# Performance work log

Hardware: AMD Instinct MI355X
Metric: run time of the kernel (lower is better)

## Reference

```python
import jax, jax.numpy as jnp
import numpy as np

B, C, Ci, H, W = 4, 256, 128, 64, 64  # batch, in_channels, inter_channels, spatial
BN_EPS = 1e-5


def setup_inputs() -> dict:
    key = jax.random.key(0)
    ks = jax.random.split(key, 8)
    s = (2.0 / C) ** 0.5  # kaiming fan_in std for 1x1 conv over C inputs
    return {
        "a": jax.random.normal(ks[0], (B, C, H, W), jnp.float32),
        "b": jax.random.normal(ks[1], (B, C, H, W), jnp.float32),
        "theta_w": jax.random.normal(ks[2], (Ci, C), jnp.float32) * s,
        "theta_b": jnp.zeros((Ci,), jnp.float32),
        "phi_w": jax.random.normal(ks[3], (Ci, C), jnp.float32) * s,
        "phi_b": jnp.zeros((Ci,), jnp.float32),
        "g_w": jax.random.normal(ks[4], (Ci, C), jnp.float32) * s,
        "g_b": jnp.zeros((Ci,), jnp.float32),
        "W_w": jax.random.normal(ks[5], (C, Ci), jnp.float32) * (2.0 / Ci) ** 0.5,
        "bn_gamma": jnp.ones((C,), jnp.float32),
        "bn_beta": jnp.zeros((C,), jnp.float32),
        "bn_mean": jnp.zeros((C,), jnp.float32),
        "bn_var": jnp.ones((C,), jnp.float32),
    }


def _conv1x1(x, w, bias=None):
    # x: [B,Cin,H,W], w: [Cout,Cin] -> [B,Cout,H,W]
    y = jnp.einsum("oc,bchw->bohw", w, x)
    if bias is not None:
        y = y + bias[None, :, None, None]
    return y


def reference(a, b, theta_w, theta_b, phi_w, phi_b, g_w, g_b, W_w,
              bn_gamma, bn_beta, bn_mean, bn_var):
    Bsz, _, h, w = a.shape
    n = h * w
    theta_a = _conv1x1(a, theta_w, theta_b).reshape(Bsz, Ci, n).transpose(0, 2, 1)  # [B,N,Ci]
    phi_b_ = _conv1x1(b, phi_w, phi_b).reshape(Bsz, Ci, n)                          # [B,Ci,N]
    f = jnp.einsum("bnc,bcm->bnm", theta_a, phi_b_) / n                             # [B,N,N]
    g_b_ = _conv1x1(b, g_w, g_b).reshape(Bsz, Ci, n).transpose(0, 2, 1)             # [B,N,Ci]
    y = jnp.einsum("bnm,bmc->bnc", f, g_b_)                                         # [B,N,Ci]
    y = y.transpose(0, 2, 1).reshape(Bsz, Ci, h, w)
    wy = _conv1x1(y, W_w)                                                           # no bias
    inv = jax.lax.rsqrt(bn_var + BN_EPS)
    out = (wy - bn_mean[None, :, None, None]) * (bn_gamma * inv)[None, :, None, None] \
          + bn_beta[None, :, None, None]
    return out
```

## Files before the change

### kernel.cpp

```cpp
#include <hip/hip_runtime.h>
#include <hip/hip_bf16.h>

#define NSP 4096
#define CCH 256
#define CIN 128
#define BN_EPS 1e-5f

typedef __bf16 bf16x8 __attribute__((ext_vector_type(8)));
typedef __bf16 bf16x4 __attribute__((ext_vector_type(4)));
typedef float f32x4 __attribute__((ext_vector_type(4)));
typedef unsigned short u16x8 __attribute__((ext_vector_type(8)));

typedef const __attribute__((address_space(1))) unsigned int gu32;
typedef __attribute__((address_space(3))) unsigned int lu32;


__device__ __forceinline__ float4 fetch_tr(const float* __restrict__ A, int lda, int m0,
                                           int k0, int tid) {
  const int r = tid >> 2, kq = (tid & 3) << 2;
  return *(const float4*)(A + (size_t)(m0 + r) * lda + k0 + kq);
}
__device__ __forceinline__ void stash_tr(float (*As)[68], float4 v, int tid) {
  const int r = tid >> 2, kq = (tid & 3) << 2;
  As[kq + 0][r] = v.x; As[kq + 1][r] = v.y; As[kq + 2][r] = v.z; As[kq + 3][r] = v.w;
}
__device__ __forceinline__ float4 fetch_dir(const float* __restrict__ B, int ldb, int k0,
                                            int n0, int tid) {
  const int kr = tid >> 4, nq = (tid & 15) << 2;
  return *(const float4*)(B + (size_t)(k0 + kr) * ldb + n0 + nq);
}
__device__ __forceinline__ void stash_dir(float (*Bs)[68], float4 v, int tid) {
  const int kr = tid >> 4, nq = (tid & 15) << 2;
  *(float4*)(&Bs[kr][nq]) = v;
}

__device__ __forceinline__ void mm16(const float (*As)[68], const float (*Bs)[68],
                                     float acc[4][4], int ty, int tx) {
#pragma unroll
  for (int kk = 0; kk < 16; ++kk) {
    const float4 av = *(const float4*)(&As[kk][ty << 2]);
    const float4 bv = *(const float4*)(&Bs[kk][tx << 2]);
    const float ar[4] = {av.x, av.y, av.z, av.w};
    const float br[4] = {bv.x, bv.y, bv.z, bv.w};
#pragma unroll
    for (int i = 0; i < 4; ++i)
#pragma unroll
      for (int j = 0; j < 4; ++j) acc[i][j] += ar[i] * br[j];
  }
}

__device__ __forceinline__ float wave_reduce(float v) {
#pragma unroll
  for (int off = 32; off; off >>= 1) v += __shfl_down(v, off);
  return v;
}

__global__ __launch_bounds__(256) void prep_kernel(
    const float* __restrict__ bin, const float* __restrict__ a,
    const float* __restrict__ W_w, const float* __restrict__ g_w,
    const float* __restrict__ phi_w, const float* __restrict__ theta_w,
    const float* __restrict__ phi_b, const float* __restrict__ theta_b,
    const float* __restrict__ g_b,
    __bf16* __restrict__ bhi, __bf16* __restrict__ blo,
    float* __restrict__ srow,
    float* __restrict__ Wg, __bf16* __restrict__ Wghi, __bf16* __restrict__ Wglo,
    __bf16* __restrict__ PTthi, __bf16* __restrict__ PTtlo,
    __bf16* __restrict__ at,
    float* __restrict__ vb_g, float* __restrict__ vpt, float* __restrict__ wgb,
    float* __restrict__ dvec) {
  __shared__ float smem[64 * 68];
  const int idx = blockIdx.x;
  const int t = threadIdx.x;
  const int wave = t >> 6, lane = t & 63;
  if (idx < 1024) {
    const int row = idx;
    const float* src = bin + (size_t)row * NSP + t * 16;
    float sum = 0.f;
    unsigned short h16[16], l16[16];
#pragma unroll
    for (int i = 0; i < 4; ++i) {
      const float4 v = *(const float4*)(src + i * 4);
      const float vv[4] = {v.x, v.y, v.z, v.w};
      sum += v.x + v.y + v.z + v.w;
#pragma unroll
      for (int e = 0; e < 4; ++e) {
        const unsigned u = __float_as_uint(vv[e]);
        h16[i * 4 + e] = (unsigned short)(u >> 16);
        const float hf = __uint_as_float(u & 0xffff0000u);
        l16[i * 4 + e] = (unsigned short)(__float_as_uint(vv[e] - hf) >> 16);
      }
    }
    unsigned short* dh = (unsigned short*)bhi + (size_t)row * NSP + t * 16;
    unsigned short* dl = (unsigned short*)blo + (size_t)row * NSP + t * 16;
    *(u16x8*)dh = *(u16x8*)&h16[0];
    *(u16x8*)(dh + 8) = *(u16x8*)&h16[8];
    *(u16x8*)dl = *(u16x8*)&l16[0];
    *(u16x8*)(dl + 8) = *(u16x8*)&l16[8];
#pragma unroll
    for (int off = 32; off; off >>= 1) sum += __shfl_down(sum, off);
    if (lane == 0) smem[wave] = sum;
    __syncthreads();
    if (t == 0) srow[row] = smem[0] + smem[1] + smem[2] + smem[3];
  } else if (idx < 2048) {
    const int p = idx - 1024;
    const int n0 = (p & 63) * 64, c0 = ((p >> 6) & 3) * 64, b = p >> 8;
    float (*tile)[68] = (float(*)[68])smem;
    const int cr = t >> 4, nq = (t & 15) << 2;
    const float* src = a + ((size_t)(b * CCH + c0)) * NSP + n0;
#pragma unroll
    for (int s = 0; s < 4; ++s) {
      const float4 v = *(const float4*)(src + (size_t)(cr + s * 16) * NSP + nq);
      *(float4*)&tile[cr + s * 16][nq] = v;
    }
    __syncthreads();
    const int n = t >> 2, cq = (t & 3) << 4;
    __bf16 outv[16];
#pragma unroll
    for (int i = 0; i < 16; ++i) outv[i] = (__bf16)tile[cq + i][n];
    __bf16* dst = at + ((size_t)(b * NSP + n0 + n)) * CCH + c0 + cq;
    *(bf16x8*)dst = *(bf16x8*)&outv[0];
    *(bf16x8*)(dst + 8) = *(bf16x8*)&outv[8];
  } else if (idx < 2080) {
    const int p = idx - 2048;
    const int zsel = p >> 4, rem = p & 15;
    const int m0 = (rem >> 2) * 64, n0 = (rem & 3) * 64;
    float (*As)[68] = (float(*)[68])smem;
    float (*Bs)[68] = (float(*)[68])(smem + 16 * 68);
    const int ty = t >> 4, tx = t & 15;
    float acc[4][4] = {};
    if (zsel == 0) {
      float4 ar = fetch_tr(W_w, CIN, m0, 0, t);
      float4 br = fetch_dir(g_w, CCH, 0, n0, t);
      for (int kt = 0; kt < 8; ++kt) {
        stash_tr(As, ar, t); stash_dir(Bs, br, t);
        __syncthreads();
        if (kt < 7) { ar = fetch_tr(W_w, CIN, m0, (kt + 1) * 16, t);
                      br = fetch_dir(g_w, CCH, (kt + 1) * 16, n0, t); }
        mm16(As, Bs, acc, ty, tx);
        __syncthreads();
      }
#pragma unroll
      for (int i = 0; i < 4; ++i) {
        const size_t off = (size_t)(m0 + (ty << 2) + i) * 256 + n0 + (tx << 2);
        *(float4*)(Wg + off) = make_float4(acc[i][0], acc[i][1], acc[i][2], acc[i][3]);
        __bf16 h4[4], l4[4];
#pragma unroll
        for (int j = 0; j < 4; ++j) {
          const __bf16 h = (__bf16)acc[i][j];
          h4[j] = h; l4[j] = (__bf16)(acc[i][j] - (float)h);
        }
        *(bf16x4*)(Wghi + off) = *(bf16x4*)h4;
        *(bf16x4*)(Wglo + off) = *(bf16x4*)l4;
      }
    } else {
      float4 ar = fetch_dir(theta_w, CCH, 0, m0, t);
      float4 br = fetch_dir(phi_w, CCH, 0, n0, t);
      for (int kt = 0; kt < 8; ++kt) {
        stash_dir(As, ar, t); stash_dir(Bs, br, t);
        __syncthreads();
        if (kt < 7) { ar = fetch_dir(theta_w, CCH, (kt + 1) * 16, m0, t);
                      br = fetch_dir(phi_w, CCH, (kt + 1) * 16, n0, t); }
        mm16(As, Bs, acc, ty, tx);
        __syncthreads();
      }
#pragma unroll
      for (int i = 0; i < 4; ++i) {
        const size_t off = (size_t)(m0 + (ty << 2) + i) * 256 + n0 + (tx << 2);
        __bf16 h4[4], l4[4];
#pragma unroll
        for (int j = 0; j < 4; ++j) {
          const __bf16 h = (__bf16)acc[i][j];
          h4[j] = h; l4[j] = (__bf16)(acc[i][j] - (float)h);
        }
        *(bf16x4*)(PTthi + off) = *(bf16x4*)h4;
        *(bf16x4*)(PTtlo + off) = *(bf16x4*)l4;
      }
    }
  } else if (idx == 2080) {
    float* tb_s = smem;
    float* pb_s = smem + 128;
    if (t < 128) { tb_s[t] = theta_b[t]; pb_s[t] = phi_b[t]; }
    __syncthreads();
    float acc = 0.f;
#pragma unroll 8
    for (int i = 0; i < 128; ++i) acc += phi_w[(size_t)i * 256 + t] * tb_s[i];
    vb_g[t] = acc;
    if (t < 64) {
      float pv = pb_s[t] * tb_s[t] + pb_s[t + 64] * tb_s[t + 64];
      pv = wave_reduce(pv);
      if (t == 0) dvec[0] = pv;
    }
  } else if (idx == 2081) {
    float* pb_s = smem;
    if (t < 128) pb_s[t] = phi_b[t];
    __syncthreads();
    float acc = 0.f;
#pragma unroll 8
    for (int i = 0; i < 128; ++i) acc += pb_s[i] * theta_w[(size_t)i * 256 + t];
    vpt[t] = acc;
  } else {
    const int p = idx - 2082;
    float* gb_s = smem;
    if (t < 128) gb_s[t] = g_b[t];
    __syncthreads();
    const float2 gv = *(const float2*)&gb_s[lane * 2];
    for (int i = 0; i < 16; ++i) {
      const int o = p * 64 + wave * 16 + i;
      const float2 r = *(const float2*)(W_w + (size_t)o * 128 + lane * 2);
      float v = fmaf(r.x, gv.x, r.y * gv.y);
      v = wave_reduce(v);
      if (lane == 0) wgb[o] = v;
    }
  }
}

__global__ __launch_bounds__(256) void gram_kernel(
    const __bf16* __restrict__ bhi, const __bf16* __restrict__ blo,
    float* __restrict__ Gpart,
    const float* __restrict__ srow, const float* __restrict__ Wg,
    const __bf16* __restrict__ PTthi, const __bf16* __restrict__ PTtlo,
    const float* __restrict__ vb_g,
    float* __restrict__ Wgs, float* __restrict__ sPTv, float* __restrict__ dvec) {
  __shared__ __bf16 At[2][64][64];
  __shared__ __bf16 Bt[2][64][64];
  const int idx = blockIdx.x;
  const int t = threadIdx.x;
  const int wave = t >> 6, lane = t & 63;
  if (idx < 512) {
    const int jt = idx & 3, it = (idx >> 2) & 3;
    const int z = idx >> 4, batch = z >> 3, kc = z & 7;
    const int m = lane & 15, q = lane >> 4;
    const size_t rowbase = (size_t)batch * CCH;
    const int colbase = kc * 512;
    const int rseg = lane >> 3, ch = lane & 7;
    const int u = ch ^ rseg;
    const int h = u >> 2, j = u & 3;
    const __bf16* gsrc = h ? blo : bhi;

    auto stage = [&](int ph, int ks) {
#pragma unroll
      for (int c = 0; c < 4; ++c) {
        const int s = wave * 4 + c;
        const int isB = s >> 3;
        const int kb = s & 7;
        const int grow = (isB ? jt : it) * 64 + kb * 8 + rseg;
        const __bf16* gp = gsrc + (rowbase + (size_t)grow) * NSP +
                           colbase + ks * 32 + j * 8;
        const __bf16* lp = isB ? &Bt[ph][kb * 8][0] : &At[ph][kb * 8][0];
        __builtin_amdgcn_global_load_lds((gu32*)(const void*)gp,
                                         (lu32*)(void*)lp, 16, 0, 0);
      }
    };

    f32x4 acc[4] = {};
    const int chA = q ^ (m & 7);
    stage(0, 0);
    int ph = 0;
    for (int ks = 0; ks < 16; ++ks) {
      __syncthreads();
      if (ks < 15) stage(ph ^ 1, ks + 1);
      const bf16x8 ah = *(const bf16x8*)&At[ph][wave * 16 + m][chA * 8];
      const bf16x8 al = *(const bf16x8*)&At[ph][wave * 16 + m][(chA ^ 4) * 8];
#pragma unroll
      for (int t4 = 0; t4 < 4; ++t4) {
        const bf16x8 bh = *(const bf16x8*)&Bt[ph][t4 * 16 + m][chA * 8];
        const bf16x8 bl = *(const bf16x8*)&Bt[ph][t4 * 16 + m][(chA ^ 4) * 8];
        acc[t4] = __builtin_amdgcn_mfma_f32_16x16x32_bf16(ah, bh, acc[t4], 0, 0, 0);
        acc[t4] = __builtin_amdgcn_mfma_f32_16x16x32_bf16(ah, bl, acc[t4], 0, 0, 0);
        acc[t4] = __builtin_amdgcn_mfma_f32_16x16x32_bf16(al, bh, acc[t4], 0, 0, 0);
      }
      ph ^= 1;
    }
    float* Gp = Gpart + ((size_t)(kc * 4 + batch)) * 65536;
#pragma unroll
    for (int t4 = 0; t4 < 4; ++t4)
#pragma unroll
      for (int r = 0; r < 4; ++r)
        Gp[(size_t)(it * 64 + wave * 16 + q * 4 + r) * 256 + jt * 64 + t4 * 16 + m] =
            acc[t4][r];
  } else {
    float* lds = (float*)&At[0][0][0];
    const int p = idx - 512;
    const int b = p >> 4, seg = p & 15;
    lds[t] = srow[b * 256 + t];
    __syncthreads();
    const float4 sv = *(const float4*)&lds[lane * 4];
    for (int i = wave; i < 16; i += 4) {
      const int o = seg * 16 + i;
      const float4 r = *(const float4*)(Wg + (size_t)o * 256 + lane * 4);
      float v = fmaf(r.x, sv.x, fmaf(r.y, sv.y, fmaf(r.z, sv.z, r.w * sv.w)));
      v = wave_reduce(v);
      if (lane == 0) Wgs[b * 256 + o] = v;
    }
    for (int i = wave; i < 16; i += 4) {
      const int c = seg * 16 + i;
      const bf16x4 ph = *(const bf16x4*)(PTthi + (size_t)c * 256 + lane * 4);
      const bf16x4 pl = *(const bf16x4*)(PTtlo + (size_t)c * 256 + lane * 4);
      const float svv[4] = {sv.x, sv.y, sv.z, sv.w};
      float v = 0.f;
#pragma unroll
      for (int e = 0; e < 4; ++e) v += ((float)ph[e] + (float)pl[e]) * svv[e];
      v = wave_reduce(v);
      if (lane == 0) sPTv[b * 256 + c] = v;
    }
    if (seg == 0 && wave == 0) {
      const float4 vbv = *(const float4*)(vb_g + lane * 4);
      float v = fmaf(vbv.x, sv.x, fmaf(vbv.y, sv.y, fmaf(vbv.z, sv.z, vbv.w * sv.w)));
      v = wave_reduce(v);
      if (lane == 0) dvec[1 + b] = v;
    }
  }
}

__global__ __launch_bounds__(256) void redw2_kernel(
    const float* __restrict__ Gpart, const float* __restrict__ vb_g,
    float* __restrict__ t2_g,
    const __bf16* __restrict__ Wghi, const __bf16* __restrict__ Wglo,
    __bf16* __restrict__ W2hi, __bf16* __restrict__ W2lo) {
  const int blk = blockIdx.x;
  const int t = threadIdx.x;
  const int wave = t >> 6, lane = t & 63;
  __shared__ __bf16 Gsh[16][264], Gsl[16][264];
  const int b = blk >> 4, nt = blk & 15;
  const int rr = t >> 4;
  const int c0 = (t & 15) * 16;
  f32x4 s[4] = {};
#pragma unroll
  for (int p = 0; p < 8; ++p) {
    const float* src = Gpart + (((size_t)(p * 4 + b)) << 16) +
                       (size_t)(nt * 16 + rr) * 256 + c0;
#pragma unroll
    for (int e = 0; e < 4; ++e) s[e] += *(const f32x4*)(src + e * 4);
  }
  {
    float part = 0.f;
#pragma unroll
    for (int e = 0; e < 4; ++e) {
      const float4 vv = *(const float4*)(vb_g + c0 + e * 4);
      part += s[e][0] * vv.x + s[e][1] * vv.y + s[e][2] * vv.z + s[e][3] * vv.w;
    }
#pragma unroll
    for (int off = 8; off; off >>= 1) part += __shfl_down(part, off);
    if ((t & 15) == 0) t2_g[b * 256 + nt * 16 + rr] = part;
  }
  __bf16 h8[16], l8[16];
#pragma unroll
  for (int e = 0; e < 16; ++e) {
    const float x = s[e >> 2][e & 3];
    const __bf16 h = (__bf16)x;
    h8[e] = h; l8[e] = (__bf16)(x - (float)h);
  }
  *(bf16x8*)&Gsh[rr][c0] = *(bf16x8*)&h8[0];
  *(bf16x8*)&Gsh[rr][c0 + 8] = *(bf16x8*)&h8[8];
  *(bf16x8*)&Gsl[rr][c0] = *(bf16x8*)&l8[0];
  *(bf16x8*)&Gsl[rr][c0 + 8] = *(bf16x8*)&l8[8];
  __syncthreads();
  const int m = lane & 15, q = lane >> 4;
  f32x4 acc[4] = {};
#pragma unroll
  for (int ks = 0; ks < 8; ++ks) {
    const int k = ks * 32 + q * 8;
    const bf16x8 bh = *(const bf16x8*)&Gsh[m][k];
    const bf16x8 bl = *(const bf16x8*)&Gsl[m][k];
#pragma unroll
    for (int i = 0; i < 4; ++i) {
      const int mt = i * 4 + wave;
      const bf16x8 ah = *(const bf16x8*)(Wghi + (size_t)(mt * 16 + m) * 256 + k);
      const bf16x8 al = *(const bf16x8*)(Wglo + (size_t)(mt * 16 + m) * 256 + k);
      acc[i] = __builtin_amdgcn_mfma_f32_16x16x32_bf16(ah, bh, acc[i], 0, 0, 0);
      acc[i] = __builtin_amdgcn_mfma_f32_16x16x32_bf16(ah, bl, acc[i], 0, 0, 0);
      acc[i] = __builtin_amdgcn_mfma_f32_16x16x32_bf16(al, bh, acc[i], 0, 0, 0);
    }
  }
#pragma unroll
  for (int i = 0; i < 4; ++i) {
    const int mt = i * 4 + wave;
#pragma unroll
    for (int r = 0; r < 4; ++r) {
      const size_t off = ((size_t)b << 16) + (size_t)(mt * 16 + q * 4 + r) * 256 +
                         nt * 16 + m;
      const float v = acc[i][r];
      const __bf16 h = (__bf16)v;
      W2hi[off] = h;
      W2lo[off] = (__bf16)(v - (float)h);
    }
  }
}

__global__ __launch_bounds__(256) void wout_mfma_kernel(
    const __bf16* __restrict__ W2hi, const __bf16* __restrict__ W2lo,
    const __bf16* __restrict__ PTthi, const __bf16* __restrict__ PTtlo,
    const float* __restrict__ Wgs, const float* __restrict__ sPT,
    const float* __restrict__ wgb, const float* __restrict__ vpt,
    const float* __restrict__ Wg, const float* __restrict__ t2_g,
    const float* __restrict__ dvec,
    const float* __restrict__ bn_gamma, const float* __restrict__ bn_beta,
    const float* __restrict__ bn_mean, const float* __restrict__ bn_var,
    __bf16* __restrict__ Whi, __bf16* __restrict__ Wlo,
    float* __restrict__ bias_out) {
  const int blk = blockIdx.x;
  const int t = threadIdx.x;
  const int wave = t >> 6, lane = t & 63;
  if (blk < 64) {
    const int batch = blk >> 4, nt = blk & 15;
    const int m = lane & 15, q = lane >> 4;
    const __bf16* bh_p = PTthi + (size_t)(nt * 16 + m) * 256;
    const __bf16* bl_p = PTtlo + (size_t)(nt * 16 + m) * 256;
    const __bf16* w2h = W2hi + (size_t)batch * 65536;
    const __bf16* w2l = W2lo + (size_t)batch * 65536;
    f32x4 acc[4] = {};
#pragma unroll
    for (int ks = 0; ks < 8; ++ks) {
      const int k = ks * 32 + q * 8;
      const bf16x8 bh = *(const bf16x8*)(bh_p + k);
      const bf16x8 bl = *(const bf16x8*)(bl_p + k);
#pragma unroll
      for (int i = 0; i < 4; ++i) {
        const int mt = i * 4 + wave;
        const bf16x8 ah = *(const bf16x8*)(w2h + (size_t)(mt * 16 + m) * 256 + k);
        const bf16x8 al = *(const bf16x8*)(w2l + (size_t)(mt * 16 + m) * 256 + k);
        acc[i] = __builtin_amdgcn_mfma_f32_16x16x32_bf16(ah, bh, acc[i], 0, 0, 0);
        acc[i] = __builtin_amdgcn_mfma_f32_16x16x32_bf16(ah, bl, acc[i], 0, 0, 0);
        acc[i] = __builtin_amdgcn_mfma_f32_16x16x32_bf16(al, bh, acc[i], 0, 0, 0);
      }
    }
    const float invN = 1.0f / 4096.0f;
    const int c = nt * 16 + m;
    const float vpt_c = vpt[c];
    const float sPT_c = sPT[batch * 256 + c];
#pragma unroll
    for (int i = 0; i < 4; ++i) {
      const int mt = i * 4 + wave;
#pragma unroll
      for (int r = 0; r < 4; ++r) {
        const int o = mt * 16 + q * 4 + r;
        const float sc = bn_gamma[o] * rsqrtf(bn_var[o] + BN_EPS);
        const float w = sc * ((acc[i][r] + Wgs[batch * 256 + o] * vpt_c + wgb[o] * sPT_c) * invN +
                              wgb[o] * vpt_c);
        const size_t off = (size_t)batch * 65536 + (size_t)o * 256 + c;
        const __bf16 h = (__bf16)w;
        Whi[off] = h;
        Wlo[off] = (__bf16)(w - (float)h);
      }
    }
  } else {
    const int p = blk - 64;
    const int b = p >> 2, quarter = p & 3;
    __shared__ float t2s[256];
    t2s[t] = t2_g[b * 256 + t];
    __syncthreads();
    const float d1 = dvec[0], d2 = dvec[1 + b];
    const float invN = 1.0f / 4096.0f;
    const float4 tv = *(const float4*)&t2s[lane * 4];
    for (int it = 0; it < 16; ++it) {
      const int o = quarter * 64 + wave * 16 + it;
      const float4 r = *(const float4*)(Wg + (size_t)o * 256 + lane * 4);
      float v = fmaf(r.x, tv.x, fmaf(r.y, tv.y, fmaf(r.z, tv.z, r.w * tv.w)));
      v = wave_reduce(v);
      if (lane == 0) {
        const float bias_full = (v + Wgs[b * 256 + o] * d1 +
                                 wgb[o] * (d2 + 4096.0f * d1)) * invN;
        const float sc = bn_gamma[o] * rsqrtf(bn_var[o] + BN_EPS);
        bias_out[b * 256 + o] = sc * (bias_full - bn_mean[o]) + bn_beta[o];
      }
    }
  }
}

__global__ __launch_bounds__(256) void out_mfma_kernel(const __bf16* __restrict__ Whi,
                                                       const __bf16* __restrict__ Wlo,
                                                       const __bf16* __restrict__ at,
                                                       const float* __restrict__ bias_out,
                                                       float* __restrict__ out) {
  const int ng = blockIdx.x, mt = blockIdx.y, b = blockIdx.z;
  const int wave = threadIdx.x >> 6, lane = threadIdx.x & 63;
  const int m = lane & 15, q = lane >> 4;
  const int o = mt * 64 + wave * 16 + m;
  const __bf16* wh = Whi + (size_t)b * 65536 + (size_t)o * 256;
  const __bf16* wl = Wlo + (size_t)b * 65536 + (size_t)o * 256;
  bf16x8 ah[8], al[8];
#pragma unroll
  for (int ks = 0; ks < 8; ++ks) {
    ah[ks] = *(const bf16x8*)(wh + ks * 32 + q * 8);
    al[ks] = *(const bf16x8*)(wl + ks * 32 + q * 8);
  }
  float bo[4];
#pragma unroll
  for (int r = 0; r < 4; ++r)
    bo[r] = bias_out[b * 256 + mt * 64 + wave * 16 + q * 4 + r];
  float* ob = out + (size_t)b * CCH * NSP;
#pragma unroll
  for (int nt4 = 0; nt4 < 2; ++nt4) {
    const __bf16* atb = at + ((size_t)b * NSP + ng * 128 + nt4 * 64) * CCH;
    f32x4 acc[4] = {};
#pragma unroll
    for (int ks = 0; ks < 8; ++ks) {
      const int k = ks * 32 + q * 8;
#pragma unroll
      for (int t4 = 0; t4 < 4; ++t4) {
        const bf16x8 bh = *(const bf16x8*)(atb + (size_t)(t4 * 16 + m) * 256 + k);
        acc[t4] = __builtin_amdgcn_mfma_f32_16x16x32_bf16(ah[ks], bh, acc[t4], 0, 0, 0);
        acc[t4] = __builtin_amdgcn_mfma_f32_16x16x32_bf16(al[ks], bh, acc[t4], 0, 0, 0);
      }
    }
#pragma unroll
    for (int r = 0; r < 4; ++r) {
      const int orow = mt * 64 + wave * 16 + q * 4 + r;
#pragma unroll
      for (int t4 = 0; t4 < 4; ++t4)
        ob[(size_t)orow * NSP + ng * 128 + nt4 * 64 + t4 * 16 + m] = acc[t4][r] + bo[r];
    }
  }
}

extern "C" void kernel_launch(void* const* d_in, const int* in_sizes, int n_in,
                              void* d_out, int out_size, void* d_ws, size_t ws_size,
                              hipStream_t stream) {
  (void)in_sizes; (void)n_in; (void)out_size; (void)ws_size;
  const float* a       = (const float*)d_in[0];
  const float* bI      = (const float*)d_in[1];
  const float* theta_w = (const float*)d_in[2];
  const float* theta_b = (const float*)d_in[3];
  const float* phi_w   = (const float*)d_in[4];
  const float* phi_b   = (const float*)d_in[5];
  const float* g_w     = (const float*)d_in[6];
  const float* g_b     = (const float*)d_in[7];
  const float* W_w     = (const float*)d_in[8];
  const float* bn_gamma= (const float*)d_in[9];
  const float* bn_beta = (const float*)d_in[10];
  const float* bn_mean = (const float*)d_in[11];
  const float* bn_var  = (const float*)d_in[12];
  float* out = (float*)d_out;
  float* ws  = (float*)d_ws;

  float* Gpart    = ws;
  float* srow     = ws + 4194304;
  float* Wg       = ws + 4195328;
  float* bias_out = ws + 4260864;
  float* Wgs      = ws + 4261888;
  float* sPTv     = ws + 4262912;
  float* wgb      = ws + 4263936;
  float* vpt      = ws + 4264192;
  float* vb_g     = ws + 4264448;
  float* t2_g     = ws + 4264704;
  float* dvec     = ws + 4265728;
  __bf16* at    = (__bf16*)(ws + 4265984);
  __bf16* Wghi  = (__bf16*)(ws + 6363136);
  __bf16* Wglo  = (__bf16*)(ws + 6395904);
  __bf16* PTthi = (__bf16*)(ws + 6428672);
  __bf16* PTtlo = (__bf16*)(ws + 6461440);
  __bf16* W2hi  = (__bf16*)(ws + 6494208);
  __bf16* W2lo  = (__bf16*)(ws + 6625280);
  __bf16* Whi   = (__bf16*)(ws + 6756352);
  __bf16* Wlo   = (__bf16*)(ws + 6887424);
  __bf16* bhi   = (__bf16*)(ws + 7018496);
  __bf16* blo   = (__bf16*)(ws + 9115648);

  prep_kernel<<<dim3(2086), dim3(256), 0, stream>>>(bI, a, W_w, g_w, phi_w, theta_w,
                                                    phi_b, theta_b, g_b,
                                                    bhi, blo, srow, Wg, Wghi, Wglo,
                                                    PTthi, PTtlo, at,
                                                    vb_g, vpt, wgb, dvec);
  gram_kernel<<<dim3(576), dim3(256), 0, stream>>>(bhi, blo, Gpart, srow, Wg,
                                                   PTthi, PTtlo, vb_g,
                                                   Wgs, sPTv, dvec);
  redw2_kernel<<<dim3(64), dim3(256), 0, stream>>>(Gpart, vb_g, t2_g,
                                                   Wghi, Wglo, W2hi, W2lo);
  wout_mfma_kernel<<<dim3(80), dim3(256), 0, stream>>>(W2hi, W2lo, PTthi, PTtlo,
                                                       Wgs, sPTv, wgb, vpt, Wg, t2_g,
                                                       dvec, bn_gamma, bn_beta, bn_mean,
                                                       bn_var, Whi, Wlo, bias_out);
  out_mfma_kernel<<<dim3(32, 4, 4), dim3(256), 0, stream>>>(Whi, Wlo, at, bias_out, out);
}
```

Measured before the change: 175.2 us.

## Exploit Gram matrix symmetry to compute only upper-triangular tiles

The Gram kernel now computes only the 10 upper-triangular 64x64 tiles of each 256x256 channel Gram matrix instead of all 16, cutting GEMM blocks from 512 to 320. Diagonal tiles load only the A operand and reuse it as B. Off-diagonal results are transposed through LDS and written to the mirrored location. This removes redundant MFMA work and global loads, at the cost of an extra LDS transpose pass with two barriers per off-diagonal block and less uniform per-block work.

```diff
diff --git a/kernel.cpp b/kernel.cpp
--- a/kernel.cpp
+++ b/kernel.cpp
@@ -13,6 +13,9 @@
 
 typedef const __attribute__((address_space(1))) unsigned int gu32;
 typedef __attribute__((address_space(3))) unsigned int lu32;
+
+__constant__ int IT10[10] = {0,0,0,0,1,1,1,2,2,3};
+__constant__ int JT10[10] = {0,1,2,3,1,2,3,2,3,3};
 
 
 __device__ __forceinline__ float4 fetch_tr(const float* __restrict__ A, int lda, int m0,
@@ -221,14 +224,19 @@
     const __bf16* __restrict__ PTthi, const __bf16* __restrict__ PTtlo,
     const float* __restrict__ vb_g,
     float* __restrict__ Wgs, float* __restrict__ sPTv, float* __restrict__ dvec) {
-  __shared__ __bf16 At[2][64][64];
-  __shared__ __bf16 Bt[2][64][64];
+  __shared__ __align__(16) __bf16 AtBt[2][2][64][64];
+  auto& At = AtBt[0];
+  auto& Bt = AtBt[1];
   const int idx = blockIdx.x;
   const int t = threadIdx.x;
   const int wave = t >> 6, lane = t & 63;
-  if (idx < 512) {
-    const int jt = idx & 3, it = (idx >> 2) & 3;
-    const int z = idx >> 4, batch = z >> 3, kc = z & 7;
+  if (idx < 320) {
+    const int kc = idx & 7;
+    const int rest = idx >> 3;
+    const int tile = rest % 10;
+    const int batch = rest / 10;
+    const int it = IT10[tile], jt = JT10[tile];
+    const bool diag = (it == jt);
     const int m = lane & 15, q = lane >> 4;
     const size_t rowbase = (size_t)batch * CCH;
     const int colbase = kc * 512;
@@ -242,6 +250,7 @@
       for (int c = 0; c < 4; ++c) {
         const int s = wave * 4 + c;
         const int isB = s >> 3;
+        if (diag && isB) continue;
         const int kb = s & 7;
         const int grow = (isB ? jt : it) * 64 + kb * 8 + rseg;
         const __bf16* gp = gsrc + (rowbase + (size_t)grow) * NSP +
@@ -261,10 +270,11 @@
       if (ks < 15) stage(ph ^ 1, ks + 1);
       const bf16x8 ah = *(const bf16x8*)&At[ph][wave * 16 + m][chA * 8];
       const bf16x8 al = *(const bf16x8*)&At[ph][wave * 16 + m][(chA ^ 4) * 8];
+      const __bf16 (*Bsrc)[64] = diag ? At[ph] : Bt[ph];
 #pragma unroll
       for (int t4 = 0; t4 < 4; ++t4) {
-        const bf16x8 bh = *(const bf16x8*)&Bt[ph][t4 * 16 + m][chA * 8];
-        const bf16x8 bl = *(const bf16x8*)&Bt[ph][t4 * 16 + m][(chA ^ 4) * 8];
+        const bf16x8 bh = *(const bf16x8*)&Bsrc[t4 * 16 + m][chA * 8];
+        const bf16x8 bl = *(const bf16x8*)&Bsrc[t4 * 16 + m][(chA ^ 4) * 8];
         acc[t4] = __builtin_amdgcn_mfma_f32_16x16x32_bf16(ah, bh, acc[t4], 0, 0, 0);
         acc[t4] = __builtin_amdgcn_mfma_f32_16x16x32_bf16(ah, bl, acc[t4], 0, 0, 0);
         acc[t4] = __builtin_amdgcn_mfma_f32_16x16x32_bf16(al, bh, acc[t4], 0, 0, 0);
@@ -278,9 +288,24 @@
       for (int r = 0; r < 4; ++r)
         Gp[(size_t)(it * 64 + wave * 16 + q * 4 + r) * 256 + jt * 64 + t4 * 16 + m] =
             acc[t4][r];
+    if (!diag) {
+      __syncthreads();
+      float* Tf = (float*)AtBt;
+#pragma unroll
+      for (int t4 = 0; t4 < 4; ++t4)
+#pragma unroll
+        for (int r = 0; r < 4; ++r)
+          Tf[(t4 * 16 + m) * 68 + wave * 16 + q * 4 + r] = acc[t4][r];
+      __syncthreads();
+      const int rr = t >> 2, cq = (t & 3) * 16;
+      float* Gpt = Gp + (size_t)(jt * 64 + rr) * 256 + it * 64 + cq;
+#pragma unroll
+      for (int i = 0; i < 4; ++i)
+        *(float4*)(Gpt + i * 4) = *(const float4*)&Tf[rr * 68 + cq + i * 4];
+    }
   } else {
-    float* lds = (float*)&At[0][0][0];
-    const int p = idx - 512;
+    float* lds = (float*)AtBt;
+    const int p = idx - 320;
     const int b = p >> 4, seg = p & 15;
     lds[t] = srow[b * 256 + t];
     __syncthreads();
@@ -561,7 +586,7 @@
                                                     bhi, blo, srow, Wg, Wghi, Wglo,
                                                     PTthi, PTtlo, at,
                                                     vb_g, vpt, wgb, dvec);
-  gram_kernel<<<dim3(576), dim3(256), 0, stream>>>(bhi, blo, Gpart, srow, Wg,
+  gram_kernel<<<dim3(384), dim3(256), 0, stream>>>(bhi, blo, Gpart, srow, Wg,
                                                    PTthi, PTtlo, vb_g,
                                                    Wgs, sPTv, dvec);
   redw2_kernel<<<dim3(64), dim3(256), 0, stream>>>(Gpart, vb_g, t2_g,
```

New measurement: 170.4 us. -2.7%, faster.
